# Kernel optimization log

Hardware: AMD Instinct MI355X
Metric: run time of the kernel (lower is better)

The kernel has to match this reference:

```python
import jax, jax.numpy as jnp
import numpy as np

N_NODES = 100000
N_EDGES = 1600000
D_IN = 128
D_OUT = 128
EPSILON = 0.0


def setup_inputs() -> dict:
    key = jax.random.key(0)
    k1, k2, k3, k4, k5 = jax.random.split(key, 5)
    indices = jax.random.randint(k1, (2, N_EDGES), 0, N_NODES, dtype=jnp.int64 if jax.config.jax_enable_x64 else jnp.int32)
    values = jax.random.uniform(k2, (N_EDGES,), dtype=jnp.float32)
    features = jax.random.normal(k3, (N_NODES, D_IN), dtype=jnp.float32)
    # Xavier-uniform linear weights, zero biases (as in init_parameters)
    lim1 = float(np.sqrt(6.0 / (D_IN + D_OUT)))
    lim2 = float(np.sqrt(6.0 / (D_OUT + D_OUT)))
    W1 = jax.random.uniform(k4, (D_IN, D_OUT), minval=-lim1, maxval=lim1, dtype=jnp.float32)
    W2 = jax.random.uniform(k5, (D_OUT, D_OUT), minval=-lim2, maxval=lim2, dtype=jnp.float32)
    b1 = jnp.zeros((D_OUT,), dtype=jnp.float32)
    b2 = jnp.zeros((D_OUT,), dtype=jnp.float32)
    return {"indices": indices, "values": values, "features": features,
            "W1": W1, "b1": b1, "W2": W2, "b2": b2}


def reference(indices, values, features, W1, b1, W2, b2):
    row, col = indices[0], indices[1]
    # SpMM: out[r] = sum_e values[e] * features[col[e]]  (sparse_adj @ features)
    messages = values[:, None] * features[col]              # [E, D_IN]
    neighbor = jax.ops.segment_sum(messages, row, num_segments=N_NODES)  # [N, D_IN]
    combined = (1.0 + EPSILON) * features + neighbor        # epsilon residual
    h = jax.nn.relu(combined @ W1 + b1)                     # Linear -> ReLU
    out = h @ W2 + b2                                       # Linear
    # dropout is identity in eval mode
    return out
```

## Files before the change

kernel.cpp:

```cpp
#include <hip/hip_runtime.h>

#define N_NODES 100000
#define N_EDGES 1600000
#define D 128
#define NB 782
#define BCAP 2560

typedef unsigned short u16;
typedef unsigned int u32;
typedef __attribute__((ext_vector_type(8))) short bf16x8;
typedef __attribute__((ext_vector_type(4))) float f32x4;

__device__ __forceinline__ u16 f2bf(float f) {
    u32 u = __float_as_uint(f);
    u += 0x7fffu + ((u >> 16) & 1u);
    return (u16)(u >> 16);
}


__global__ void convert_feat(const float4* __restrict__ f4, uint4* __restrict__ o4) {
    int idx = blockIdx.x * blockDim.x + threadIdx.x;
    float4 a = f4[idx * 2], b = f4[idx * 2 + 1];
    uint4 o;
    o.x = (u32)f2bf(a.x) | ((u32)f2bf(a.y) << 16);
    o.y = (u32)f2bf(a.z) | ((u32)f2bf(a.w) << 16);
    o.z = (u32)f2bf(b.x) | ((u32)f2bf(b.y) << 16);
    o.w = (u32)f2bf(b.z) | ((u32)f2bf(b.w) << 16);
    o4[idx] = o;
}

__global__ void convert_w(const float* __restrict__ W1, const float* __restrict__ W2,
                          u16* __restrict__ W1t, u16* __restrict__ W2t) {
    int flat = blockIdx.x * blockDim.x + threadIdx.x;
    int m = flat >> 14;
    int idx = flat & 16383;
    int n = idx & 127;
    int k = idx >> 7;
    const float* src = m ? W2 : W1;
    u16* dst = m ? W2t : W1t;
    dst[n * 128 + k] = f2bf(src[k * 128 + n]);
}


__global__ __launch_bounds__(256) void bin_pass(const int* __restrict__ row,
                                                const int* __restrict__ col,
                                                const float* __restrict__ val,
                                                int* __restrict__ bucketCount,
                                                int2* __restrict__ binned) {
    __shared__ int hist[NB];
    __shared__ int lbase[NB];
    int t = threadIdx.x;
    for (int i = t; i < NB; i += 256) hist[i] = 0;
    __syncthreads();
    int base = blockIdx.x * 4096;
    int r[16];
#pragma unroll
    for (int i = 0; i < 16; ++i) {
        int e = base + i * 256 + t;
        r[i] = (e < N_EDGES) ? row[e] : -1;
        if (r[i] >= 0) atomicAdd(&hist[r[i] >> 7], 1);
    }
    __syncthreads();
    for (int i = t; i < NB; i += 256) {
        int c = hist[i];
        lbase[i] = c ? atomicAdd(&bucketCount[i], c) : 0;
    }
    __syncthreads();
    for (int i = t; i < NB; i += 256) hist[i] = 0;
    __syncthreads();
#pragma unroll
    for (int i = 0; i < 16; ++i) {
        if (r[i] < 0) continue;
        int e = base + i * 256 + t;
        int bkt = r[i] >> 7;
        int pos = bkt * BCAP + lbase[bkt] + atomicAdd(&hist[bkt], 1);
        int2 ev;
        ev.x = col[e] | ((r[i] & 127) << 17);
        ev.y = __float_as_int(val[e]);
        binned[pos] = ev;
    }
}

__global__ __launch_bounds__(256) void bucket_sort(const int2* __restrict__ binned,
                                                   const int* __restrict__ bucketCount,
                                                   int2* __restrict__ rowRange,
                                                   int2* __restrict__ scev) {
    __shared__ int h[128];
    __shared__ int cur[128];
    int b = blockIdx.x, t = threadIdx.x;
    int row0 = b << 7;
    int nrows = N_NODES - row0;
    if (nrows > 128) nrows = 128;
    if (t < 128) h[t] = 0;
    __syncthreads();
    int lo = b * BCAP;
    int hi = lo + bucketCount[b];
    for (int i = lo + t; i < hi; i += 256)
        atomicAdd(&h[((u32)binned[i].x) >> 17], 1);
    __syncthreads();
    if (t < 128) cur[t] = h[t];
    __syncthreads();
    for (int d = 1; d < 128; d <<= 1) {
        int x = 0;
        if (t < 128 && t >= d) x = cur[t - d];
        __syncthreads();
        if (t < 128) cur[t] += x;
        __syncthreads();
    }
    if (t < 128) {
        int excl = lo + cur[t] - h[t];
        if (t < nrows) rowRange[row0 + t] = make_int2(excl, excl + h[t]);
        cur[t] = excl;
    }
    __syncthreads();
    for (int i = lo + t; i < hi; i += 256) {
        int2 ev = binned[i];
        int rl = ((u32)ev.x) >> 17;
        int pos = atomicAdd(&cur[rl], 1);
        scev[pos] = make_int2(ev.x & 0x1FFFF, ev.y);
    }
}


__global__ __launch_bounds__(256) void spmm_bf16(
    const int2* __restrict__ scev, const int2* __restrict__ rowRange,
    const u32* __restrict__ featb, u32* __restrict__ Xb) {
    int wid0 = (blockIdx.x * blockDim.x + threadIdx.x) >> 6;
    int wid = __builtin_amdgcn_readfirstlane(wid0);
    int lane = threadIdx.x & 63;
    if (wid >= N_NODES) return;
    int2 rr = rowRange[wid];
    int j = rr.x, end = rr.y;
    u32 self = featb[wid * 64 + lane];
    float ax0 = __uint_as_float(self << 16);
    float ay0 = __uint_as_float(self & 0xffff0000u);
    float ax1 = 0.f, ay1 = 0.f;
    for (; j + 16 <= end; j += 16) {
        int2 e[16];
        u32 p[16];
#pragma unroll
        for (int u = 0; u < 16; ++u) e[u] = scev[j + u];
#pragma unroll
        for (int u = 0; u < 16; ++u) p[u] = featb[e[u].x * 64 + lane];
#pragma unroll
        for (int u = 0; u < 16; ++u) {
            float v = __int_as_float(e[u].y);
            float lo = __uint_as_float(p[u] << 16);
            float hi = __uint_as_float(p[u] & 0xffff0000u);
            if (u & 1) {
                ax1 += v * lo;
                ay1 += v * hi;
            } else {
                ax0 += v * lo;
                ay0 += v * hi;
            }
        }
    }
    for (; j + 4 <= end; j += 4) {
        int2 e[4];
        u32 p[4];
#pragma unroll
        for (int u = 0; u < 4; ++u) e[u] = scev[j + u];
#pragma unroll
        for (int u = 0; u < 4; ++u) p[u] = featb[e[u].x * 64 + lane];
#pragma unroll
        for (int u = 0; u < 4; ++u) {
            float v = __int_as_float(e[u].y);
            float lo = __uint_as_float(p[u] << 16);
            float hi = __uint_as_float(p[u] & 0xffff0000u);
            if (u & 1) {
                ax1 += v * lo;
                ay1 += v * hi;
            } else {
                ax0 += v * lo;
                ay0 += v * hi;
            }
        }
    }
    for (; j < end; ++j) {
        int2 e = scev[j];
        float v = __int_as_float(e.y);
        u32 p = featb[e.x * 64 + lane];
        ax0 += v * __uint_as_float(p << 16);
        ay0 += v * __uint_as_float(p & 0xffff0000u);
    }
    float accx = ax0 + ax1;
    float accy = ay0 + ay1;
    Xb[wid * 64 + lane] = (u32)f2bf(accx) | ((u32)f2bf(accy) << 16);
}


template <int RELU, int OUT32>
__global__ __launch_bounds__(256, 2) void gemm_mfma(
    const u16* __restrict__ Xb, const u16* __restrict__ Wt,
    const float* __restrict__ bias, u16* __restrict__ outb, float* __restrict__ outf) {
    __shared__ u16 Ws[128][136];
    int t = threadIdx.x;
    {
        const uint4* wsrc = (const uint4*)Wt;
#pragma unroll
        for (int i = 0; i < 8; ++i) {
            int f = t + 256 * i;
            int n = f >> 4;
            int c8 = (f & 15) << 3;
            *(uint4*)&Ws[n][c8] = wsrc[f];
        }
    }
    __syncthreads();

    int w = t >> 6, lane = t & 63;
    int quad = lane >> 4, l16 = lane & 15;
    int row0 = blockIdx.x * 128 + w * 32;

    f32x4 acc[2][8];
#pragma unroll
    for (int rt = 0; rt < 2; ++rt)
#pragma unroll
        for (int ct = 0; ct < 8; ++ct) acc[rt][ct] = (f32x4){0.f, 0.f, 0.f, 0.f};

    int ra = row0 + l16;
    int rb = row0 + 16 + l16;
    if (ra > N_NODES - 1) ra = N_NODES - 1;
    if (rb > N_NODES - 1) rb = N_NODES - 1;
    const u16* pa = Xb + (size_t)ra * D + quad * 8;
    const u16* pb = Xb + (size_t)rb * D + quad * 8;

#pragma unroll
    for (int kb = 0; kb < 128; kb += 32) {
        bf16x8 a0 = *(const bf16x8*)(pa + kb);
        bf16x8 a1 = *(const bf16x8*)(pb + kb);
#pragma unroll
        for (int ct = 0; ct < 8; ++ct) {
            bf16x8 b = *(const bf16x8*)&Ws[ct * 16 + l16][kb + quad * 8];
            acc[0][ct] = __builtin_amdgcn_mfma_f32_16x16x32_bf16(a0, b, acc[0][ct], 0, 0, 0);
            acc[1][ct] = __builtin_amdgcn_mfma_f32_16x16x32_bf16(a1, b, acc[1][ct], 0, 0, 0);
        }
    }

    float bv[8];
#pragma unroll
    for (int ct = 0; ct < 8; ++ct) bv[ct] = bias[ct * 16 + l16];

#pragma unroll
    for (int rt = 0; rt < 2; ++rt) {
#pragma unroll
        for (int r = 0; r < 4; ++r) {
            int row = row0 + rt * 16 + quad * 4 + r;
            if (row >= N_NODES) continue;
#pragma unroll
            for (int ct = 0; ct < 8; ++ct) {
                float v = acc[rt][ct][r] + bv[ct];
                if (RELU) v = fmaxf(v, 0.f);
                int col = ct * 16 + l16;
                if (OUT32) outf[(size_t)row * D + col] = v;
                else outb[(size_t)row * D + col] = f2bf(v);
            }
        }
    }
}

extern "C" void kernel_launch(void* const* d_in, const int* in_sizes, int n_in,
                              void* d_out, int out_size, void* d_ws, size_t ws_size,
                              hipStream_t stream) {
    const int* indices = (const int*)d_in[0];
    const float* values = (const float*)d_in[1];
    const float* features = (const float*)d_in[2];
    const float* W1 = (const float*)d_in[3];
    const float* b1 = (const float*)d_in[4];
    const float* W2 = (const float*)d_in[5];
    const float* b2 = (const float*)d_in[6];

    const int* row = indices;
    const int* col = indices + N_EDGES;

    int* wsI = (int*)d_ws;
    int* bucketCount = wsI;
    int2* rowRange = (int2*)(wsI + 784);
    int2* scev = (int2*)(wsI + 784 + 2 * N_NODES);
    u32* featb = (u32*)(wsI + 784 + 2 * N_NODES + 2 * NB * BCAP);
    u16* Hb = (u16*)featb;
    u16* W1t = (u16*)(featb + (size_t)N_NODES * 64);
    u16* W2t = W1t + 16384;

    int2* binned = (int2*)d_out;
    u32* Xb = (u32*)((char*)d_out + (size_t)N_NODES * D * 2);
    float* outf = (float*)d_out;

    hipMemsetAsync(bucketCount, 0, NB * sizeof(int), stream);

    convert_feat<<<N_NODES * D / 8 / 256, 256, 0, stream>>>((const float4*)features, (uint4*)featb);
    convert_w<<<128, 256, 0, stream>>>(W1, W2, W1t, W2t);

    int cb = (N_EDGES + 4095) / 4096;
    bin_pass<<<cb, 256, 0, stream>>>(row, col, values, bucketCount, binned);
    bucket_sort<<<NB, 256, 0, stream>>>(binned, bucketCount, rowRange, scev);

    spmm_bf16<<<(N_NODES * 64 + 255) / 256, 256, 0, stream>>>(scev, rowRange, featb, Xb);

    int gb = (N_NODES + 127) / 128;
    gemm_mfma<1, 0><<<gb, 256, 0, stream>>>((const u16*)Xb, W1t, b1, Hb, nullptr);
    gemm_mfma<0, 1><<<gb, 256, 0, stream>>>(Hb, W2t, b2, nullptr, outf);
}
```

Before: 290.4 us.

## Merge prep kernels, fuse both GEMMs via LDS, and pad SpMM tail loop

Three preprocessing kernels (feature conversion, weight transpose, edge binning) are merged into one launch, with work chosen by block index. This removes launch gaps and lets the independent work overlap. The two dense layers are fused into one kernel: the ReLU hidden tile is staged in LDS (reusing the weight buffer) and multiplied by W2 read from global, so the hidden matrix never makes a round trip through HBM. The SpMM tail loops are replaced by a padded 16-wide loop with zero weights, and the workspace and output buffers are reassigned so featb and Xb do not collide.

Measured after the change: 291.4 us. About the same (+0.3%).

```diff
diff --git a/kernel.cpp b/kernel.cpp
--- a/kernel.cpp
+++ b/kernel.cpp
@@ -18,41 +18,50 @@
 }
 
 
-__global__ void convert_feat(const float4* __restrict__ f4, uint4* __restrict__ o4) {
-    int idx = blockIdx.x * blockDim.x + threadIdx.x;
-    float4 a = f4[idx * 2], b = f4[idx * 2 + 1];
-    uint4 o;
-    o.x = (u32)f2bf(a.x) | ((u32)f2bf(a.y) << 16);
-    o.y = (u32)f2bf(a.z) | ((u32)f2bf(a.w) << 16);
-    o.z = (u32)f2bf(b.x) | ((u32)f2bf(b.y) << 16);
-    o.w = (u32)f2bf(b.z) | ((u32)f2bf(b.w) << 16);
-    o4[idx] = o;
-}
-
-__global__ void convert_w(const float* __restrict__ W1, const float* __restrict__ W2,
-                          u16* __restrict__ W1t, u16* __restrict__ W2t) {
-    int flat = blockIdx.x * blockDim.x + threadIdx.x;
-    int m = flat >> 14;
-    int idx = flat & 16383;
-    int n = idx & 127;
-    int k = idx >> 7;
-    const float* src = m ? W2 : W1;
-    u16* dst = m ? W2t : W1t;
-    dst[n * 128 + k] = f2bf(src[k * 128 + n]);
-}
-
-
-__global__ __launch_bounds__(256) void bin_pass(const int* __restrict__ row,
-                                                const int* __restrict__ col,
-                                                const float* __restrict__ val,
-                                                int* __restrict__ bucketCount,
-                                                int2* __restrict__ binned) {
+#define CF_BLKS 6250
+#define CW_BLKS 128
+#define BIN_BLKS 391
+
+__global__ __launch_bounds__(256) void prep(
+    const float* __restrict__ features, u32* __restrict__ featb,
+    const float* __restrict__ W1, const float* __restrict__ W2,
+    u16* __restrict__ W1t, u16* __restrict__ W2t,
+    const int* __restrict__ row, const int* __restrict__ col,
+    const float* __restrict__ val,
+    int* __restrict__ bucketCount, int2* __restrict__ binned) {
     __shared__ int hist[NB];
     __shared__ int lbase[NB];
+    int bid = blockIdx.x;
     int t = threadIdx.x;
+
+    if (bid < CF_BLKS) {
+        int idx = bid * 256 + t;
+        const float4* f4 = (const float4*)features;
+        float4 a = f4[idx * 2], b = f4[idx * 2 + 1];
+        uint4 o;
+        o.x = (u32)f2bf(a.x) | ((u32)f2bf(a.y) << 16);
+        o.y = (u32)f2bf(a.z) | ((u32)f2bf(a.w) << 16);
+        o.z = (u32)f2bf(b.x) | ((u32)f2bf(b.y) << 16);
+        o.w = (u32)f2bf(b.z) | ((u32)f2bf(b.w) << 16);
+        ((uint4*)featb)[idx] = o;
+        return;
+    }
+    if (bid < CF_BLKS + CW_BLKS) {
+        int flat = (bid - CF_BLKS) * 256 + t;
+        int m = flat >> 14;
+        int idx = flat & 16383;
+        int n = idx & 127;
+        int k = idx >> 7;
+        const float* src = m ? W2 : W1;
+        u16* dst = m ? W2t : W1t;
+        dst[n * 128 + k] = f2bf(src[k * 128 + n]);
+        return;
+    }
+
+    int b = bid - (CF_BLKS + CW_BLKS);
     for (int i = t; i < NB; i += 256) hist[i] = 0;
     __syncthreads();
-    int base = blockIdx.x * 4096;
+    int base = b * 4096;
     int r[16];
 #pragma unroll
     for (int i = 0; i < 16; ++i) {
@@ -135,11 +144,16 @@
     float ax0 = __uint_as_float(self << 16);
     float ay0 = __uint_as_float(self & 0xffff0000u);
     float ax1 = 0.f, ay1 = 0.f;
-    for (; j + 16 <= end; j += 16) {
+    for (; j < end; j += 16) {
         int2 e[16];
         u32 p[16];
 #pragma unroll
-        for (int u = 0; u < 16; ++u) e[u] = scev[j + u];
+        for (int u = 0; u < 16; ++u) {
+            int idx = j + u;
+            int c = (idx < end) ? idx : (end - 1);
+            e[u] = scev[c];
+            if (idx >= end) e[u].y = 0;
+        }
 #pragma unroll
         for (int u = 0; u < 16; ++u) p[u] = featb[e[u].x * 64 + lane];
 #pragma unroll
@@ -156,54 +170,26 @@
             }
         }
     }
-    for (; j + 4 <= end; j += 4) {
-        int2 e[4];
-        u32 p[4];
-#pragma unroll
-        for (int u = 0; u < 4; ++u) e[u] = scev[j + u];
-#pragma unroll
-        for (int u = 0; u < 4; ++u) p[u] = featb[e[u].x * 64 + lane];
-#pragma unroll
-        for (int u = 0; u < 4; ++u) {
-            float v = __int_as_float(e[u].y);
-            float lo = __uint_as_float(p[u] << 16);
-            float hi = __uint_as_float(p[u] & 0xffff0000u);
-            if (u & 1) {
-                ax1 += v * lo;
-                ay1 += v * hi;
-            } else {
-                ax0 += v * lo;
-                ay0 += v * hi;
-            }
-        }
-    }
-    for (; j < end; ++j) {
-        int2 e = scev[j];
-        float v = __int_as_float(e.y);
-        u32 p = featb[e.x * 64 + lane];
-        ax0 += v * __uint_as_float(p << 16);
-        ay0 += v * __uint_as_float(p & 0xffff0000u);
-    }
     float accx = ax0 + ax1;
     float accy = ay0 + ay1;
     Xb[wid * 64 + lane] = (u32)f2bf(accx) | ((u32)f2bf(accy) << 16);
 }
 
 
-template <int RELU, int OUT32>
-__global__ __launch_bounds__(256, 2) void gemm_mfma(
-    const u16* __restrict__ Xb, const u16* __restrict__ Wt,
-    const float* __restrict__ bias, u16* __restrict__ outb, float* __restrict__ outf) {
+__global__ __launch_bounds__(256, 2) void gemm_fused(
+    const u16* __restrict__ Xb, const u16* __restrict__ W1t,
+    const float* __restrict__ b1, const u16* __restrict__ W2t,
+    const float* __restrict__ b2, float* __restrict__ outf) {
     __shared__ u16 Ws[128][136];
+    u16(*Ht)[130] = (u16(*)[130]) & Ws[0][0];
+
     int t = threadIdx.x;
     {
-        const uint4* wsrc = (const uint4*)Wt;
+        const uint4* wsrc = (const uint4*)W1t;
 #pragma unroll
         for (int i = 0; i < 8; ++i) {
             int f = t + 256 * i;
-            int n = f >> 4;
-            int c8 = (f & 15) << 3;
-            *(uint4*)&Ws[n][c8] = wsrc[f];
+            *(uint4*)&Ws[f >> 4][(f & 15) << 3] = wsrc[f];
         }
     }
     __syncthreads();
@@ -237,9 +223,53 @@
         }
     }
 
-    float bv[8];
-#pragma unroll
-    for (int ct = 0; ct < 8; ++ct) bv[ct] = bias[ct * 16 + l16];
+    float bv1[8];
+#pragma unroll
+    for (int ct = 0; ct < 8; ++ct) bv1[ct] = b1[ct * 16 + l16];
+
+    __syncthreads();
+
+    int hbase = w * 32;
+#pragma unroll
+    for (int rt = 0; rt < 2; ++rt) {
+#pragma unroll
+        for (int ct = 0; ct < 8; ++ct) {
+            float v0 = fmaxf(acc[rt][ct][0] + bv1[ct], 0.f);
+            float v1 = fmaxf(acc[rt][ct][1] + bv1[ct], 0.f);
+            float v2 = fmaxf(acc[rt][ct][2] + bv1[ct], 0.f);
+            float v3 = fmaxf(acc[rt][ct][3] + bv1[ct], 0.f);
+            u16* dst = &Ht[ct * 16 + l16][hbase + rt * 16 + quad * 4];
+            ((u32*)dst)[0] = (u32)f2bf(v0) | ((u32)f2bf(v1) << 16);
+            ((u32*)dst)[1] = (u32)f2bf(v2) | ((u32)f2bf(v3) << 16);
+        }
+    }
+    __syncthreads();
+
+    f32x4 acc2[2][8];
+#pragma unroll
+    for (int rt = 0; rt < 2; ++rt)
+#pragma unroll
+        for (int ct = 0; ct < 8; ++ct) acc2[rt][ct] = (f32x4){0.f, 0.f, 0.f, 0.f};
+
+#pragma unroll
+    for (int kb = 0; kb < 128; kb += 32) {
+        bf16x8 a0, a1;
+#pragma unroll
+        for (int i = 0; i < 8; ++i) {
+            a0[i] = (short)Ht[kb + quad * 8 + i][hbase + l16];
+            a1[i] = (short)Ht[kb + quad * 8 + i][hbase + 16 + l16];
+        }
+#pragma unroll
+        for (int ct = 0; ct < 8; ++ct) {
+            bf16x8 b = *(const bf16x8*)(W2t + (size_t)(ct * 16 + l16) * D + kb + quad * 8);
+            acc2[0][ct] = __builtin_amdgcn_mfma_f32_16x16x32_bf16(a0, b, acc2[0][ct], 0, 0, 0);
+            acc2[1][ct] = __builtin_amdgcn_mfma_f32_16x16x32_bf16(a1, b, acc2[1][ct], 0, 0, 0);
+        }
+    }
+
+    float bv2[8];
+#pragma unroll
+    for (int ct = 0; ct < 8; ++ct) bv2[ct] = b2[ct * 16 + l16];
 
 #pragma unroll
     for (int rt = 0; rt < 2; ++rt) {
@@ -249,11 +279,7 @@
             if (row >= N_NODES) continue;
 #pragma unroll
             for (int ct = 0; ct < 8; ++ct) {
-                float v = acc[rt][ct][r] + bv[ct];
-                if (RELU) v = fmaxf(v, 0.f);
-                int col = ct * 16 + l16;
-                if (OUT32) outf[(size_t)row * D + col] = v;
-                else outb[(size_t)row * D + col] = f2bf(v);
+                outf[(size_t)row * D + ct * 16 + l16] = acc2[rt][ct][r] + bv2[ct];
             }
         }
     }
@@ -277,27 +303,23 @@
     int* bucketCount = wsI;
     int2* rowRange = (int2*)(wsI + 784);
     int2* scev = (int2*)(wsI + 784 + 2 * N_NODES);
-    u32* featb = (u32*)(wsI + 784 + 2 * N_NODES + 2 * NB * BCAP);
-    u16* Hb = (u16*)featb;
-    u16* W1t = (u16*)(featb + (size_t)N_NODES * 64);
+    u32* Xb = (u32*)(wsI + 784 + 2 * N_NODES + 2 * NB * BCAP);
+    u16* W1t = (u16*)(Xb + (size_t)N_NODES * 64);
     u16* W2t = W1t + 16384;
 
     int2* binned = (int2*)d_out;
-    u32* Xb = (u32*)((char*)d_out + (size_t)N_NODES * D * 2);
+    u32* featb = (u32*)((char*)d_out + (size_t)N_NODES * D * 2);
     float* outf = (float*)d_out;
 
     hipMemsetAsync(bucketCount, 0, NB * sizeof(int), stream);
 
-    convert_feat<<<N_NODES * D / 8 / 256, 256, 0, stream>>>((const float4*)features, (uint4*)featb);
-    convert_w<<<128, 256, 0, stream>>>(W1, W2, W1t, W2t);
-
-    int cb = (N_EDGES + 4095) / 4096;
-    bin_pass<<<cb, 256, 0, stream>>>(row, col, values, bucketCount, binned);
+    prep<<<CF_BLKS + CW_BLKS + BIN_BLKS, 256, 0, stream>>>(
+        features, featb, W1, W2, W1t, W2t, row, col, values, bucketCount, binned);
+
     bucket_sort<<<NB, 256, 0, stream>>>(binned, bucketCount, rowRange, scev);
 
     spmm_bf16<<<(N_NODES * 64 + 255) / 256, 256, 0, stream>>>(scev, rowRange, featb, Xb);
 
-    int gb = (N_NODES + 127) / 128;
-    gemm_mfma<1, 0><<<gb, 256, 0, stream>>>((const u16*)Xb, W1t, b1, Hb, nullptr);
-    gemm_mfma<0, 1><<<gb, 256, 0, stream>>>(Hb, W2t, b2, nullptr, outf);
-}
+    gemm_fused<<<(N_NODES + 127) / 128, 256, 0, stream>>>(
+        (const u16*)Xb, W1t, b1, W2t, b2, outf);
+}
```
